# Optimization experiments

Measured on AMD Instinct MI355X. Metric: run time of the kernel, lower is better.

The kernel has to match this reference:

```python
import jax, jax.numpy as jnp
import numpy as np

B, N, C = 64, 8192, 64
C4 = C // 4
EPS_BN = 1e-5


def setup_inputs() -> dict:
    key = jax.random.key(0)
    ks = jax.random.split(key, 12)
    s = 0.05
    return {
        "x": jax.random.normal(ks[0], (B, N, 10), jnp.float32),
        "y": jax.random.normal(ks[1], (B, N, 13), jnp.float32),
        "W_l": jax.random.normal(ks[2], (10, C), jnp.float32) * s,
        "b_l": jax.random.normal(ks[3], (C,), jnp.float32) * s,
        "W_r": jax.random.normal(ks[4], (13, C), jnp.float32) * s,
        "b_r": jax.random.normal(ks[5], (C,), jnp.float32) * s,
        "W_qk": jax.random.normal(ks[6], (C4, C), jnp.float32) * s,  # shared q/k 1x1-conv weight
        "W_v": jax.random.normal(ks[7], (C, C), jnp.float32) * s,
        "b_v": jax.random.normal(ks[8], (C,), jnp.float32) * s,
        "W_t": jax.random.normal(ks[9], (C, C), jnp.float32) * s,
        "b_t": jax.random.normal(ks[10], (C,), jnp.float32) * s,
        "gamma": jnp.ones((C,), jnp.float32),
        "beta": jnp.zeros((C,), jnp.float32),
    }


def reference(x, y, W_l, b_l, W_r, b_r, W_qk, W_v, b_v, W_t, b_t, gamma, beta):
    # x: [B,N,10] -> linear_l; y: [B,N,13] -> linear_r  (torch keeps [B,C,N]; we keep [B,N,C])
    X = x @ W_l + b_l                                   # [B,N,C]
    Y = y @ W_r + b_r                                   # [B,N,C]
    # 1x1 convs == per-point matmuls; attention runs ACROSS the batch dim per point n
    xq = jnp.einsum('bnc,dc->nbd', X, W_qk)             # [N,B,C/4]
    yk = jnp.einsum('bnc,dc->nbd', Y, W_qk)             # [N,B,C/4] (shared weight)
    yv = jnp.einsum('bnc,dc->nbd', Y, W_v) + b_v        # [N,B,C]
    energy = jnp.einsum('nbd,ned->nbe', xq, yk)         # [N,B,B]
    attn = jax.nn.softmax(energy, axis=-1)
    # extra L1 renormalization over dim=1 (offset-attention style)
    attn = attn / (1e-9 + attn.sum(axis=1, keepdims=True))
    yr = jnp.einsum('nbe,nec->bnc', attn, yv)           # [B,N,C]
    # trans_conv -> BatchNorm (training-mode batch stats) -> ReLU -> residual -> max over points
    t = jnp.einsum('bnc,dc->bnd', X - yr, W_t) + b_t    # [B,N,C]
    mean = t.mean(axis=(0, 1))
    var = t.var(axis=(0, 1))                            # biased var, as BN uses
    tn = gamma * (t - mean) * jax.lax.rsqrt(var + EPS_BN) + beta
    xres = X + jax.nn.relu(tn)                          # [B,N,C]
    return jnp.max(xres, axis=1)[:, :, None]            # [B,C,1] to match torch layout
```

## Files before the change

### kernel.cpp

```cpp
#include <hip/hip_runtime.h>
#include <hip/hip_bf16.h>

#define B_ 64
#define N_ 8192
#define C_ 64

using short8 = __attribute__((ext_vector_type(8))) short;
using f32x4  = __attribute__((ext_vector_type(4))) float;

#define MFMA16(a, b, c) __builtin_amdgcn_mfma_f32_16x16x32_bf16((a), (b), (c), 0, 0, 0)

__device__ inline unsigned short f2bf(float f) {
  union { float f; unsigned int u; } v; v.f = f;
  unsigned int r = v.u + 0x7FFFu + ((v.u >> 16) & 1u);
  return (unsigned short)(r >> 16);
}


__global__ void k0_prep(const float* __restrict__ W_l, const float* __restrict__ b_l,
                        const float* __restrict__ W_r, const float* __restrict__ b_r,
                        const float* __restrict__ W_qk, const float* __restrict__ W_v,
                        const float* __restrict__ b_v, const float* __restrict__ W_t,
                        float* __restrict__ wsf) {
  const int tid = threadIdx.x;
  float* b_lq_ = wsf + 33920;
  float* b_rk_ = wsf + 33936;
  float* b_rv_ = wsf + 33952;
  unsigned short* wb = (unsigned short*)(wsf + 34016);
  unsigned short* BLQ = wb;
  unsigned short* BRK = wb + 512;
  unsigned short* BL  = wb + 1024;
  unsigned short* BRV = wb + 3072;
  unsigned short* BT  = wb + 5120;
  if (blockIdx.x == 0) {
    for (int i = tid; i < 512; i += 256) {
      int d = i >> 5, kk = i & 31;
      unsigned short o = 0;
      if (kk < 10) {
        float s = 0.f;
        for (int c = 0; c < 64; ++c) s = fmaf(W_l[kk * 64 + c], W_qk[d * 64 + c], s);
        o = f2bf(s);
      }
      BLQ[i] = o;
    }
    for (int i = tid; i < 512; i += 256) {
      int d = i >> 5, kk = i & 31, k = kk - 16;
      unsigned short o = 0;
      if (k >= 0 && k < 13) {
        float s = 0.f;
        for (int c = 0; c < 64; ++c) s = fmaf(W_r[k * 64 + c], W_qk[d * 64 + c], s);
        o = f2bf(s);
      }
      BRK[i] = o;
    }
    if (tid < 32) {
      int d = tid & 15;
      const float* bb = (tid < 16) ? b_l : b_r;
      float s = 0.f;
      for (int c = 0; c < 64; ++c) s = fmaf(bb[c], W_qk[d * 64 + c], s);
      ((tid < 16) ? b_lq_ : b_rk_)[d] = s;
    }
  } else if (blockIdx.x == 1) {
    for (int i = tid; i < 2048; i += 256) {
      int c = i >> 5, kk = i & 31, k = kk - 16;
      unsigned short o = 0;
      if (k >= 0 && k < 13) {
        float s = 0.f;
        for (int j = 0; j < 64; ++j) s = fmaf(W_r[k * 64 + j], W_v[c * 64 + j], s);
        o = f2bf(s);
      }
      BRV[i] = o;
    }
    if (tid < 64) {
      float s = b_v[tid];
      for (int j = 0; j < 64; ++j) s = fmaf(b_r[j], W_v[tid * 64 + j], s);
      b_rv_[tid] = s;
    }
  } else if (blockIdx.x == 2) {
    for (int i = tid; i < 2048; i += 256) {
      int c = i >> 5, kk = i & 31;
      BL[i] = (kk < 10) ? f2bf(W_l[kk * 64 + c]) : (unsigned short)0;
    }
    for (int i = tid; i < 1024; i += 256) wsf[i] = 0.f;
  } else {
    for (int i = tid; i < 4096; i += 256) BT[i] = f2bf(W_t[i]);
  }
}

__global__ __launch_bounds__(256, 4)
void k1_attn(const float* __restrict__ x, const float* __restrict__ y,
             const float* __restrict__ wsf,
             const float* __restrict__ b_l, const float* __restrict__ b_t,
             float* __restrict__ stats) {
  __shared__ __align__(16) short Axy[64 * 40];
  __shared__ __align__(16) short xkA[64 * 24];
  __shared__ __align__(16) short ykB[64 * 24];
  __shared__ __align__(16) short yvT[64 * 72];
  __shared__ __align__(16) short aZ[4 * 2304];
  __shared__ float scr[512];

  const float* b_lq_ = wsf + 33920;
  const float* b_rk_ = wsf + 33936;
  const float* b_rv_ = wsf + 33952;
  const unsigned short* wbase = (const unsigned short*)(wsf + 34016);
  const unsigned short* BLQ = wbase;
  const unsigned short* BRK = wbase + 512;
  const unsigned short* BL  = wbase + 1024;
  const unsigned short* BRV = wbase + 3072;
  const unsigned short* BT  = wbase + 5120;
  unsigned short* tg = (unsigned short*)(wsf + 34016) + 9216;

  const int n    = blockIdx.x;
  const int tid  = threadIdx.x;
  const int w    = tid >> 6;
  const int lane = tid & 63;
  const int l15  = lane & 15;
  const int q    = lane >> 4;
  const int r0   = w * 16;
  short* const aw = aZ + w * 2304;
  short* const Zw = aw + 1152;

  {
    const int b = tid >> 2, i = tid & 3;
    const float* xp = x + ((size_t)b * N_ + n) * 10;
    const float* yp = y + ((size_t)b * N_ + n) * 13;
    short* Ar = Axy + b * 40;
    Ar[i]      = (short)f2bf(xp[i]);
    Ar[i + 4]  = (short)f2bf(xp[i + 4]);
    Ar[i + 8]  = (i + 8 < 10) ? (short)f2bf(xp[i + 8]) : (short)0;
    Ar[12 + i] = 0;
    Ar[16 + i]      = (short)f2bf(yp[i]);
    Ar[20 + i]      = (short)f2bf(yp[i + 4]);
    Ar[24 + i]      = (short)f2bf(yp[i + 8]);
    Ar[28 + i]      = (i + 12 < 13) ? (short)f2bf(yp[i + 12]) : (short)0;
  }
  __syncthreads();

  const short8 aA = *(const short8*)&Axy[(r0 + l15) * 40 + q * 8];

  f32x4 xq, yk, X[4], yv[4];
  {
    const short8 bq = *(const short8*)&BLQ[l15 * 32 + q * 8];
    const float bl1 = b_lq_[l15];
    xq = MFMA16(aA, bq, ((f32x4){bl1, bl1, bl1, bl1}));
    const short8 bk = *(const short8*)&BRK[l15 * 32 + q * 8];
    const float bk1 = b_rk_[l15];
    yk = MFMA16(aA, bk, ((f32x4){bk1, bk1, bk1, bk1}));
  }
#pragma unroll
  for (int f = 0; f < 4; ++f) {
    const int c = f * 16 + l15;
    const short8 bl = *(const short8*)&BL[c * 32 + q * 8];
    const float bX = b_l[c];
    X[f] = MFMA16(aA, bl, ((f32x4){bX, bX, bX, bX}));
    const short8 bv = *(const short8*)&BRV[c * 32 + q * 8];
    const float bV = b_rv_[c];
    yv[f] = MFMA16(aA, bv, ((f32x4){bV, bV, bV, bV}));
  }
#pragma unroll
  for (int j = 0; j < 4; ++j) {
    xkA[(r0 + q * 4 + j) * 24 + l15] = (short)f2bf(xq[j]);
    ykB[(r0 + q * 4 + j) * 24 + l15] = (short)f2bf(yk[j]);
  }
#pragma unroll
  for (int f = 0; f < 4; ++f)
#pragma unroll
    for (int j = 0; j < 4; ++j)
      yvT[(f * 16 + l15) * 72 + (r0 + q * 4 + j)] = (short)f2bf(yv[f][j]);
  __syncthreads();

  const short8 z8 = (short8)(short)0;
  const short8 aq = (q < 2) ? *(const short8*)&xkA[(r0 + l15) * 24 + q * 8] : z8;
  f32x4 E[4];
#pragma unroll
  for (int f = 0; f < 4; ++f) {
    const short8 bk = (q < 2) ? *(const short8*)&ykB[(f * 16 + l15) * 24 + q * 8] : z8;
    E[f] = MFMA16(aq, bk, ((f32x4){0.f, 0.f, 0.f, 0.f}));
  }

  float inv_r[4];
#pragma unroll
  for (int j = 0; j < 4; ++j) {
    float s = 0.f;
#pragma unroll
    for (int f = 0; f < 4; ++f) { E[f][j] = __expf(E[f][j]); s += E[f][j]; }
    s += __shfl_xor(s, 1);
    s += __shfl_xor(s, 2);
    s += __shfl_xor(s, 4);
    s += __shfl_xor(s, 8);
    inv_r[j] = 1.0f / s;
  }
#pragma unroll
  for (int f = 0; f < 4; ++f) {
    float cs = E[f][0] * inv_r[0] + E[f][1] * inv_r[1] + E[f][2] * inv_r[2] + E[f][3] * inv_r[3];
    cs += __shfl_xor(cs, 16);
    cs += __shfl_xor(cs, 32);
    if (lane < 16) scr[w * 64 + f * 16 + l15] = cs;
  }
  __syncthreads();
  float csvv[4];
#pragma unroll
  for (int f = 0; f < 4; ++f) {
    const int col = f * 16 + l15;
    csvv[f] = 1.0f / (1e-9f + scr[col] + scr[64 + col] + scr[128 + col] + scr[192 + col]);
  }
#pragma unroll
  for (int f = 0; f < 4; ++f)
#pragma unroll
    for (int j = 0; j < 4; ++j)
      aw[(q * 4 + j) * 72 + f * 16 + l15] = (short)f2bf(E[f][j] * inv_r[j] * csvv[f]);

  const short8 aA0 = *(const short8*)&aw[l15 * 72 + q * 8];
  const short8 aA1 = *(const short8*)&aw[l15 * 72 + 32 + q * 8];
#pragma unroll
  for (int f = 0; f < 4; ++f) {
    const short8 b0 = *(const short8*)&yvT[(f * 16 + l15) * 72 + q * 8];
    const short8 b1 = *(const short8*)&yvT[(f * 16 + l15) * 72 + 32 + q * 8];
    f32x4 yr = MFMA16(aA0, b0, ((f32x4){0.f, 0.f, 0.f, 0.f}));
    yr = MFMA16(aA1, b1, yr);
#pragma unroll
    for (int j = 0; j < 4; ++j)
      Zw[(q * 4 + j) * 72 + f * 16 + l15] = (short)f2bf(X[f][j] - yr[j]);
  }

  const short8 aZ0 = *(const short8*)&Zw[l15 * 72 + q * 8];
  const short8 aZ1 = *(const short8*)&Zw[l15 * 72 + 32 + q * 8];
  unsigned short* tp = tg + (size_t)n * 4096;
  f32x4 t[4];
#pragma unroll
  for (int f = 0; f < 4; ++f) {
    const int c = f * 16 + l15;
    const short8 bt0 = *(const short8*)&BT[c * 64 + q * 8];
    const short8 bt1 = *(const short8*)&BT[c * 64 + 32 + q * 8];
    const float bT = b_t[c];
    t[f] = MFMA16(aZ0, bt0, ((f32x4){bT, bT, bT, bT}));
    t[f] = MFMA16(aZ1, bt1, t[f]);
#pragma unroll
    for (int j = 0; j < 4; ++j)
      tp[(r0 + q * 4 + j) * 64 + c] = f2bf(t[f][j]);
  }
  __syncthreads();
#pragma unroll
  for (int f = 0; f < 4; ++f) {
    float s = 0.f, ss = 0.f;
#pragma unroll
    for (int j = 0; j < 4; ++j) { s += t[f][j]; ss = fmaf(t[f][j], t[f][j], ss); }
    s  += __shfl_xor(s, 16);  s  += __shfl_xor(s, 32);
    ss += __shfl_xor(ss, 16); ss += __shfl_xor(ss, 32);
    if (lane < 16) {
      scr[w * 64 + f * 16 + l15]       = s;
      scr[256 + w * 64 + f * 16 + l15] = ss;
    }
  }
  __syncthreads();
  if (tid < 64) {
    const float s  = scr[tid] + scr[64 + tid] + scr[128 + tid] + scr[192 + tid];
    const float ss = scr[256 + tid] + scr[320 + tid] + scr[384 + tid] + scr[448 + tid];
    float* st = stats + (n & 7) * 128;
    atomicAdd(&st[tid], s);
    atomicAdd(&st[64 + tid], ss);
  }
}

__global__ void k2_stats(const float* __restrict__ stats, float* __restrict__ meanr) {
  const int c = threadIdx.x;
  if (c < 64) {
    float s = 0.f, ss = 0.f;
    for (int r = 0; r < 8; ++r) { s += stats[r * 128 + c]; ss += stats[r * 128 + 64 + c]; }
    const float inv = 1.0f / (float)(B_ * N_);
    const float mu = s * inv;
    const float var = fmaf(ss, inv, -mu * mu);
    meanr[c] = mu;
    meanr[64 + c] = rsqrtf(var + 1e-5f);
  }
}

__global__ __launch_bounds__(256)
void k3_max(const float* __restrict__ x, const float* __restrict__ W_l,
            const float* __restrict__ b_l, const float* __restrict__ gamma,
            const float* __restrict__ beta, const unsigned short* __restrict__ tg,
            const float* __restrict__ meanr, float* __restrict__ pmax)
{
  const int b = blockIdx.x >> 3;
  const int chunk = blockIdx.x & 7;
  const int c = threadIdx.x & 63;
  const int sub = threadIdx.x >> 6;
  float wl[10];
#pragma unroll
  for (int k = 0; k < 10; ++k) wl[k] = W_l[k * 64 + c];
  const float bl = b_l[c];
  const float g = gamma[c], be = beta[c];
  const float mu = meanr[c], rs = meanr[64 + c];
  float m = -1e30f;
  const int nbase = chunk * 1024 + sub;
  for (int j = 0; j < 256; ++j) {
    const int n = nbase + j * 4;
    const float* xp = x + ((size_t)b * N_ + n) * 10;
    float X = bl;
#pragma unroll
    for (int k = 0; k < 10; ++k) X = fmaf(xp[k], wl[k], X);
    union { unsigned int u; float f; } tv;
    tv.u = ((unsigned int)tg[(size_t)n * 4096 + b * 64 + c]) << 16;
    const float tn = fmaf(g * (tv.f - mu), rs, be);
    m = fmaxf(m, X + fmaxf(tn, 0.f));
  }
  __shared__ float sm[4][64];
  sm[sub][c] = m;
  __syncthreads();
  if (threadIdx.x < 64) {
    const float r = fmaxf(fmaxf(sm[0][c], sm[1][c]), fmaxf(sm[2][c], sm[3][c]));
    pmax[(size_t)blockIdx.x * 64 + c] = r;
  }
}

__global__ void k4_final(const float* __restrict__ pmax, float* __restrict__ out) {
  const int b = blockIdx.x, c = threadIdx.x;
  float m = -1e30f;
  for (int ch = 0; ch < 8; ++ch) m = fmaxf(m, pmax[((size_t)b * 8 + ch) * 64 + c]);
  out[b * 64 + c] = m;
}

extern "C" void kernel_launch(void* const* d_in, const int* in_sizes, int n_in,
                              void* d_out, int out_size, void* d_ws, size_t ws_size,
                              hipStream_t stream) {
  const float* x     = (const float*)d_in[0];
  const float* y     = (const float*)d_in[1];
  const float* W_l   = (const float*)d_in[2];
  const float* b_l   = (const float*)d_in[3];
  const float* W_r   = (const float*)d_in[4];
  const float* b_r   = (const float*)d_in[5];
  const float* W_qk  = (const float*)d_in[6];
  const float* W_v   = (const float*)d_in[7];
  const float* b_v   = (const float*)d_in[8];
  const float* W_t   = (const float*)d_in[9];
  const float* b_t   = (const float*)d_in[10];
  const float* gamma = (const float*)d_in[11];
  const float* beta  = (const float*)d_in[12];
  float* out = (float*)d_out;

  float* wsf = (float*)d_ws;
  float* stats = wsf;
  float* meanr = wsf + 1024;
  float* pmax  = wsf + 1152;
  unsigned short* tg = (unsigned short*)(wsf + 34016) + 9216;

  hipLaunchKernelGGL(k0_prep, dim3(4), dim3(256), 0, stream,
                     W_l, b_l, W_r, b_r, W_qk, W_v, b_v, W_t, wsf);
  hipLaunchKernelGGL(k1_attn, dim3(N_), dim3(256), 0, stream,
                     x, y, wsf, b_l, b_t, stats);
  hipLaunchKernelGGL(k2_stats, dim3(1), dim3(64), 0, stream, stats, meanr);
  hipLaunchKernelGGL(k3_max, dim3(512), dim3(256), 0, stream,
                     x, W_l, b_l, gamma, beta, tg, meanr, pmax);
  hipLaunchKernelGGL(k4_final, dim3(64), dim3(64), 0, stream, pmax, out);
}
```

Measured before the change: 248.9 us.

## Fold q/k weights into bilinear matrix, reassociate value path, transpose t layout

The attention kernel now computes the energy through a precomputed bilinear matrix (W_l·W_qk)(W_r·W_qk)^T with biases folded in as a ones column. The value path is reassociated as (attn·Y)·(W_r W_v) instead of materialising yv, which removes several MFMAs and LDS transposes. The t buffer is stored batch-major so the max kernel can read contiguous vectorized bf16 runs, and that kernel processes four channels per lane with folded BN constants over twice as many blocks. It also switches to cheaper round-half-up bf16 conversion and raises the occupancy hint, at the cost of slightly different rounding and extra bf16 quantisation of intermediate products.

```diff
diff --git a/kernel.cpp b/kernel.cpp
--- a/kernel.cpp
+++ b/kernel.cpp
@@ -1,9 +1,7 @@
 #include <hip/hip_runtime.h>
-#include <hip/hip_bf16.h>
 
 #define B_ 64
 #define N_ 8192
-#define C_ 64
 
 using short8 = __attribute__((ext_vector_type(8))) short;
 using f32x4  = __attribute__((ext_vector_type(4))) float;
@@ -12,8 +10,11 @@
 
 __device__ inline unsigned short f2bf(float f) {
   union { float f; unsigned int u; } v; v.f = f;
-  unsigned int r = v.u + 0x7FFFu + ((v.u >> 16) & 1u);
-  return (unsigned short)(r >> 16);
+  return (unsigned short)((v.u + 0x8000u) >> 16);
+}
+__device__ inline float bf2f(unsigned int hi16_in_low) {
+  union { unsigned int u; float f; } v; v.u = hi16_in_low << 16;
+  return v.f;
 }
 
 
@@ -23,63 +24,60 @@
                         const float* __restrict__ b_v, const float* __restrict__ W_t,
                         float* __restrict__ wsf) {
   const int tid = threadIdx.x;
-  float* b_lq_ = wsf + 33920;
-  float* b_rk_ = wsf + 33936;
-  float* b_rv_ = wsf + 33952;
-  unsigned short* wb = (unsigned short*)(wsf + 34016);
-  unsigned short* BLQ = wb;
-  unsigned short* BRK = wb + 512;
-  unsigned short* BL  = wb + 1024;
-  unsigned short* BRV = wb + 3072;
-  unsigned short* BT  = wb + 5120;
+  unsigned short* wb   = (unsigned short*)(wsf + 66688);
+  unsigned short* BM   = wb;
+  unsigned short* BL   = wb + 512;
+  unsigned short* BRV2 = wb + 2560;
+  unsigned short* BT   = wb + 4608;
   if (blockIdx.x == 0) {
-    for (int i = tid; i < 512; i += 256) {
-      int d = i >> 5, kk = i & 31;
+    __shared__ float Wlq[11 * 16], Wrk[14 * 16];
+    for (int idx = tid; idx < 11 * 16; idx += 256) {
+      int i = idx >> 4, d = idx & 15;
+      const float* a = (i < 10) ? (W_l + i * 64) : b_l;
+      float s = 0.f;
+      for (int c = 0; c < 64; ++c) s = fmaf(a[c], W_qk[d * 64 + c], s);
+      Wlq[idx] = s;
+    }
+    for (int idx = tid; idx < 14 * 16; idx += 256) {
+      int j = idx >> 4, d = idx & 15;
+      const float* a = (j < 13) ? (W_r + j * 64) : b_r;
+      float s = 0.f;
+      for (int c = 0; c < 64; ++c) s = fmaf(a[c], W_qk[d * 64 + c], s);
+      Wrk[idx] = s;
+    }
+    __syncthreads();
+    for (int idx = tid; idx < 512; idx += 256) {
+      int j = idx >> 5, kk = idx & 31;
       unsigned short o = 0;
-      if (kk < 10) {
+      if (j < 14 && kk < 11) {
         float s = 0.f;
-        for (int c = 0; c < 64; ++c) s = fmaf(W_l[kk * 64 + c], W_qk[d * 64 + c], s);
+        for (int d = 0; d < 16; ++d) s = fmaf(Wlq[kk * 16 + d], Wrk[j * 16 + d], s);
         o = f2bf(s);
       }
-      BLQ[i] = o;
-    }
-    for (int i = tid; i < 512; i += 256) {
-      int d = i >> 5, kk = i & 31, k = kk - 16;
+      BM[idx] = o;
+    }
+  } else if (blockIdx.x == 1) {
+    for (int idx = tid; idx < 2048; idx += 256) {
+      int c = idx >> 5, kk = idx & 31;
       unsigned short o = 0;
-      if (k >= 0 && k < 13) {
+      if (kk < 13) {
         float s = 0.f;
-        for (int c = 0; c < 64; ++c) s = fmaf(W_r[k * 64 + c], W_qk[d * 64 + c], s);
+        for (int j = 0; j < 64; ++j) s = fmaf(W_r[kk * 64 + j], W_v[c * 64 + j], s);
+        o = f2bf(s);
+      } else if (kk == 13) {
+        float s = b_v[c];
+        for (int j = 0; j < 64; ++j) s = fmaf(b_r[j], W_v[c * 64 + j], s);
         o = f2bf(s);
       }
-      BRK[i] = o;
-    }
-    if (tid < 32) {
-      int d = tid & 15;
-      const float* bb = (tid < 16) ? b_l : b_r;
-      float s = 0.f;
-      for (int c = 0; c < 64; ++c) s = fmaf(bb[c], W_qk[d * 64 + c], s);
-      ((tid < 16) ? b_lq_ : b_rk_)[d] = s;
-    }
-  } else if (blockIdx.x == 1) {
-    for (int i = tid; i < 2048; i += 256) {
-      int c = i >> 5, kk = i & 31, k = kk - 16;
+      BRV2[idx] = o;
+    }
+  } else if (blockIdx.x == 2) {
+    for (int idx = tid; idx < 2048; idx += 256) {
+      int c = idx >> 5, kk = idx & 31;
       unsigned short o = 0;
-      if (k >= 0 && k < 13) {
-        float s = 0.f;
-        for (int j = 0; j < 64; ++j) s = fmaf(W_r[k * 64 + j], W_v[c * 64 + j], s);
-        o = f2bf(s);
-      }
-      BRV[i] = o;
-    }
-    if (tid < 64) {
-      float s = b_v[tid];
-      for (int j = 0; j < 64; ++j) s = fmaf(b_r[j], W_v[tid * 64 + j], s);
-      b_rv_[tid] = s;
-    }
-  } else if (blockIdx.x == 2) {
-    for (int i = tid; i < 2048; i += 256) {
-      int c = i >> 5, kk = i & 31;
-      BL[i] = (kk < 10) ? f2bf(W_l[kk * 64 + c]) : (unsigned short)0;
+      if (kk < 10) o = f2bf(W_l[kk * 64 + c]);
+      else if (kk == 10) o = f2bf(b_l[c]);
+      BL[idx] = o;
     }
     for (int i = tid; i < 1024; i += 256) wsf[i] = 0.f;
   } else {
@@ -87,28 +85,22 @@
   }
 }
 
-__global__ __launch_bounds__(256, 4)
+__global__ __launch_bounds__(256, 6)
 void k1_attn(const float* __restrict__ x, const float* __restrict__ y,
-             const float* __restrict__ wsf,
-             const float* __restrict__ b_l, const float* __restrict__ b_t,
+             const float* __restrict__ wsf, const float* __restrict__ b_t,
              float* __restrict__ stats) {
   __shared__ __align__(16) short Axy[64 * 40];
-  __shared__ __align__(16) short xkA[64 * 24];
-  __shared__ __align__(16) short ykB[64 * 24];
-  __shared__ __align__(16) short yvT[64 * 72];
-  __shared__ __align__(16) short aZ[4 * 2304];
+  __shared__ __align__(16) short YT[16 * 72];
+  __shared__ __align__(16) short awZ[4 * 1152];
+  __shared__ __align__(16) short GU[4 * 256];
   __shared__ float scr[512];
 
-  const float* b_lq_ = wsf + 33920;
-  const float* b_rk_ = wsf + 33936;
-  const float* b_rv_ = wsf + 33952;
-  const unsigned short* wbase = (const unsigned short*)(wsf + 34016);
-  const unsigned short* BLQ = wbase;
-  const unsigned short* BRK = wbase + 512;
-  const unsigned short* BL  = wbase + 1024;
-  const unsigned short* BRV = wbase + 3072;
-  const unsigned short* BT  = wbase + 5120;
-  unsigned short* tg = (unsigned short*)(wsf + 34016) + 9216;
+  const unsigned short* wb   = (const unsigned short*)(wsf + 66688);
+  const unsigned short* BM   = wb;
+  const unsigned short* BL   = wb + 512;
+  const unsigned short* BRV2 = wb + 2560;
+  const unsigned short* BT   = wb + 4608;
+  unsigned short* tg = (unsigned short*)(wsf + 66688) + 8704;
 
   const int n    = blockIdx.x;
   const int tid  = threadIdx.x;
@@ -117,65 +109,53 @@
   const int l15  = lane & 15;
   const int q    = lane >> 4;
   const int r0   = w * 16;
-  short* const aw = aZ + w * 2304;
-  short* const Zw = aw + 1152;
+  short* const aw = awZ + w * 1152;
+  short* const gu = GU + w * 256;
 
   {
     const int b = tid >> 2, i = tid & 3;
     const float* xp = x + ((size_t)b * N_ + n) * 10;
     const float* yp = y + ((size_t)b * N_ + n) * 13;
     short* Ar = Axy + b * 40;
-    Ar[i]      = (short)f2bf(xp[i]);
-    Ar[i + 4]  = (short)f2bf(xp[i + 4]);
-    Ar[i + 8]  = (i + 8 < 10) ? (short)f2bf(xp[i + 8]) : (short)0;
-    Ar[12 + i] = 0;
-    Ar[16 + i]      = (short)f2bf(yp[i]);
-    Ar[20 + i]      = (short)f2bf(yp[i + 4]);
-    Ar[24 + i]      = (short)f2bf(yp[i + 8]);
-    Ar[28 + i]      = (i + 12 < 13) ? (short)f2bf(yp[i + 12]) : (short)0;
-  }
-  __syncthreads();
-
+    Ar[i]     = (short)f2bf(xp[i]);
+    Ar[i + 4] = (short)f2bf(xp[i + 4]);
+    short v8 = 0;
+    if (i < 2) v8 = (short)f2bf(xp[i + 8]);
+    else if (i == 2) v8 = (short)0x3F80;
+    Ar[i + 8]  = v8;
+    Ar[i + 12] = 0;
+    const short y0 = (short)f2bf(yp[i]);
+    const short y1 = (short)f2bf(yp[i + 4]);
+    const short y2 = (short)f2bf(yp[i + 8]);
+    short y3 = 0;
+    if (i == 0) y3 = (short)f2bf(yp[12]);
+    else if (i == 1) y3 = (short)0x3F80;
+    Ar[16 + i] = y0;  Ar[20 + i] = y1;  Ar[24 + i] = y2;  Ar[28 + i] = y3;
+    YT[i * 72 + b] = y0;  YT[(i + 4) * 72 + b] = y1;
+    YT[(i + 8) * 72 + b] = y2;  YT[(i + 12) * 72 + b] = y3;
+  }
+  __syncthreads();
+
+  const short8 z8 = {0, 0, 0, 0, 0, 0, 0, 0};
+  const f32x4 zero4 = {0.f, 0.f, 0.f, 0.f};
   const short8 aA = *(const short8*)&Axy[(r0 + l15) * 40 + q * 8];
 
-  f32x4 xq, yk, X[4], yv[4];
-  {
-    const short8 bq = *(const short8*)&BLQ[l15 * 32 + q * 8];
-    const float bl1 = b_lq_[l15];
-    xq = MFMA16(aA, bq, ((f32x4){bl1, bl1, bl1, bl1}));
-    const short8 bk = *(const short8*)&BRK[l15 * 32 + q * 8];
-    const float bk1 = b_rk_[l15];
-    yk = MFMA16(aA, bk, ((f32x4){bk1, bk1, bk1, bk1}));
-  }
-#pragma unroll
-  for (int f = 0; f < 4; ++f) {
-    const int c = f * 16 + l15;
-    const short8 bl = *(const short8*)&BL[c * 32 + q * 8];
-    const float bX = b_l[c];
-    X[f] = MFMA16(aA, bl, ((f32x4){bX, bX, bX, bX}));
-    const short8 bv = *(const short8*)&BRV[c * 32 + q * 8];
-    const float bV = b_rv_[c];
-    yv[f] = MFMA16(aA, bv, ((f32x4){bV, bV, bV, bV}));
-  }
-#pragma unroll
-  for (int j = 0; j < 4; ++j) {
-    xkA[(r0 + q * 4 + j) * 24 + l15] = (short)f2bf(xq[j]);
-    ykB[(r0 + q * 4 + j) * 24 + l15] = (short)f2bf(yk[j]);
-  }
+  f32x4 G = MFMA16(aA, *(const short8*)&BM[l15 * 32 + q * 8], zero4);
+  f32x4 X[4];
 #pragma unroll
   for (int f = 0; f < 4; ++f)
-#pragma unroll
-    for (int j = 0; j < 4; ++j)
-      yvT[(f * 16 + l15) * 72 + (r0 + q * 4 + j)] = (short)f2bf(yv[f][j]);
-  __syncthreads();
-
-  const short8 z8 = (short8)(short)0;
-  const short8 aq = (q < 2) ? *(const short8*)&xkA[(r0 + l15) * 24 + q * 8] : z8;
+    X[f] = MFMA16(aA, *(const short8*)&BL[(f * 16 + l15) * 32 + q * 8], zero4);
+#pragma unroll
+  for (int j = 0; j < 4; ++j) gu[(q * 4 + j) * 16 + l15] = (short)f2bf(G[j]);
+
+  short8 aG = z8;
+  if (q < 2) aG = *(const short8*)&gu[l15 * 16 + q * 8];
   f32x4 E[4];
 #pragma unroll
   for (int f = 0; f < 4; ++f) {
-    const short8 bk = (q < 2) ? *(const short8*)&ykB[(f * 16 + l15) * 24 + q * 8] : z8;
-    E[f] = MFMA16(aq, bk, ((f32x4){0.f, 0.f, 0.f, 0.f}));
+    short8 bk = z8;
+    if (q < 2) bk = *(const short8*)&Axy[(f * 16 + l15) * 40 + 16 + q * 8];
+    E[f] = MFMA16(aG, bk, zero4);
   }
 
   float inv_r[4];
@@ -212,32 +192,34 @@
 
   const short8 aA0 = *(const short8*)&aw[l15 * 72 + q * 8];
   const short8 aA1 = *(const short8*)&aw[l15 * 72 + 32 + q * 8];
-#pragma unroll
-  for (int f = 0; f < 4; ++f) {
-    const short8 b0 = *(const short8*)&yvT[(f * 16 + l15) * 72 + q * 8];
-    const short8 b1 = *(const short8*)&yvT[(f * 16 + l15) * 72 + 32 + q * 8];
-    f32x4 yr = MFMA16(aA0, b0, ((f32x4){0.f, 0.f, 0.f, 0.f}));
-    yr = MFMA16(aA1, b1, yr);
+
+  f32x4 U = MFMA16(aA0, *(const short8*)&YT[l15 * 72 + q * 8], zero4);
+  U = MFMA16(aA1, *(const short8*)&YT[l15 * 72 + 32 + q * 8], U);
+#pragma unroll
+  for (int j = 0; j < 4; ++j) gu[(q * 4 + j) * 16 + l15] = (short)f2bf(U[j]);
+  short8 aU = z8;
+  if (q < 2) aU = *(const short8*)&gu[l15 * 16 + q * 8];
+
+#pragma unroll
+  for (int f = 0; f < 4; ++f) {
+    f32x4 yr = MFMA16(aU, *(const short8*)&BRV2[(f * 16 + l15) * 32 + q * 8], zero4);
 #pragma unroll
     for (int j = 0; j < 4; ++j)
-      Zw[(q * 4 + j) * 72 + f * 16 + l15] = (short)f2bf(X[f][j] - yr[j]);
-  }
-
-  const short8 aZ0 = *(const short8*)&Zw[l15 * 72 + q * 8];
-  const short8 aZ1 = *(const short8*)&Zw[l15 * 72 + 32 + q * 8];
-  unsigned short* tp = tg + (size_t)n * 4096;
+      aw[(q * 4 + j) * 72 + f * 16 + l15] = (short)f2bf(X[f][j] - yr[j]);
+  }
+
+  const short8 aZ0 = *(const short8*)&aw[l15 * 72 + q * 8];
+  const short8 aZ1 = *(const short8*)&aw[l15 * 72 + 32 + q * 8];
   f32x4 t[4];
 #pragma unroll
   for (int f = 0; f < 4; ++f) {
     const int c = f * 16 + l15;
-    const short8 bt0 = *(const short8*)&BT[c * 64 + q * 8];
-    const short8 bt1 = *(const short8*)&BT[c * 64 + 32 + q * 8];
     const float bT = b_t[c];
-    t[f] = MFMA16(aZ0, bt0, ((f32x4){bT, bT, bT, bT}));
-    t[f] = MFMA16(aZ1, bt1, t[f]);
+    t[f] = MFMA16(aZ0, *(const short8*)&BT[c * 64 + q * 8], ((f32x4){bT, bT, bT, bT}));
+    t[f] = MFMA16(aZ1, *(const short8*)&BT[c * 64 + 32 + q * 8], t[f]);
 #pragma unroll
     for (int j = 0; j < 4; ++j)
-      tp[(r0 + q * 4 + j) * 64 + c] = f2bf(t[f][j]);
+      tg[(size_t)(r0 + q * 4 + j) * (N_ * 64) + (size_t)n * 64 + c] = f2bf(t[f][j]);
   }
   __syncthreads();
 #pragma unroll
@@ -281,42 +263,63 @@
             const float* __restrict__ beta, const unsigned short* __restrict__ tg,
             const float* __restrict__ meanr, float* __restrict__ pmax)
 {
-  const int b = blockIdx.x >> 3;
-  const int chunk = blockIdx.x & 7;
-  const int c = threadIdx.x & 63;
-  const int sub = threadIdx.x >> 6;
-  float wl[10];
-#pragma unroll
-  for (int k = 0; k < 10; ++k) wl[k] = W_l[k * 64 + c];
-  const float bl = b_l[c];
-  const float g = gamma[c], be = beta[c];
-  const float mu = meanr[c], rs = meanr[64 + c];
-  float m = -1e30f;
-  const int nbase = chunk * 1024 + sub;
-  for (int j = 0; j < 256; ++j) {
-    const int n = nbase + j * 4;
+  const int b = blockIdx.x >> 4;
+  const int chunk = blockIdx.x & 15;
+  const int wv = threadIdx.x >> 6;
+  const int lane = threadIdx.x & 63;
+  const int c0 = (lane & 15) * 4;
+  const int nsub = lane >> 4;
+  float4 wl4[10];
+#pragma unroll
+  for (int k = 0; k < 10; ++k) wl4[k] = *(const float4*)&W_l[k * 64 + c0];
+  const float4 bl  = *(const float4*)&b_l[c0];
+  const float4 g   = *(const float4*)&gamma[c0];
+  const float4 be  = *(const float4*)&beta[c0];
+  const float4 mu  = *(const float4*)&meanr[c0];
+  const float4 rs  = *(const float4*)&meanr[64 + c0];
+  float4 grs, bmb;
+  grs.x = g.x * rs.x; grs.y = g.y * rs.y; grs.z = g.z * rs.z; grs.w = g.w * rs.w;
+  bmb.x = be.x - mu.x * grs.x; bmb.y = be.y - mu.y * grs.y;
+  bmb.z = be.z - mu.z * grs.z; bmb.w = be.w - mu.w * grs.w;
+  float4 m = {-1e30f, -1e30f, -1e30f, -1e30f};
+  const size_t tgb = (size_t)b << 19;
+  const int n0 = chunk * 512 + wv * 128 + nsub;
+  for (int jj = 0; jj < 32; ++jj) {
+    const int n = n0 + jj * 4;
+    const uint2 tv = *(const uint2*)&tg[tgb + (size_t)n * 64 + c0];
     const float* xp = x + ((size_t)b * N_ + n) * 10;
-    float X = bl;
-#pragma unroll
-    for (int k = 0; k < 10; ++k) X = fmaf(xp[k], wl[k], X);
-    union { unsigned int u; float f; } tv;
-    tv.u = ((unsigned int)tg[(size_t)n * 4096 + b * 64 + c]) << 16;
-    const float tn = fmaf(g * (tv.f - mu), rs, be);
-    m = fmaxf(m, X + fmaxf(tn, 0.f));
-  }
+    float4 X = bl;
+#pragma unroll
+    for (int k = 0; k < 10; ++k) {
+      const float xk = xp[k];
+      X.x = fmaf(xk, wl4[k].x, X.x); X.y = fmaf(xk, wl4[k].y, X.y);
+      X.z = fmaf(xk, wl4[k].z, X.z); X.w = fmaf(xk, wl4[k].w, X.w);
+    }
+    const float t0 = bf2f(tv.x & 0xFFFFu), t1 = bf2f(tv.x >> 16);
+    const float t2 = bf2f(tv.y & 0xFFFFu), t3 = bf2f(tv.y >> 16);
+    m.x = fmaxf(m.x, X.x + fmaxf(fmaf(t0, grs.x, bmb.x), 0.f));
+    m.y = fmaxf(m.y, X.y + fmaxf(fmaf(t1, grs.y, bmb.y), 0.f));
+    m.z = fmaxf(m.z, X.z + fmaxf(fmaf(t2, grs.z, bmb.z), 0.f));
+    m.w = fmaxf(m.w, X.w + fmaxf(fmaf(t3, grs.w, bmb.w), 0.f));
+  }
+  m.x = fmaxf(m.x, __shfl_xor(m.x, 16)); m.y = fmaxf(m.y, __shfl_xor(m.y, 16));
+  m.z = fmaxf(m.z, __shfl_xor(m.z, 16)); m.w = fmaxf(m.w, __shfl_xor(m.w, 16));
+  m.x = fmaxf(m.x, __shfl_xor(m.x, 32)); m.y = fmaxf(m.y, __shfl_xor(m.y, 32));
+  m.z = fmaxf(m.z, __shfl_xor(m.z, 32)); m.w = fmaxf(m.w, __shfl_xor(m.w, 32));
   __shared__ float sm[4][64];
-  sm[sub][c] = m;
+  if (lane < 16) *(float4*)&sm[wv][c0] = m;
   __syncthreads();
   if (threadIdx.x < 64) {
-    const float r = fmaxf(fmaxf(sm[0][c], sm[1][c]), fmaxf(sm[2][c], sm[3][c]));
-    pmax[(size_t)blockIdx.x * 64 + c] = r;
+    const float r = fmaxf(fmaxf(sm[0][threadIdx.x], sm[1][threadIdx.x]),
+                          fmaxf(sm[2][threadIdx.x], sm[3][threadIdx.x]));
+    pmax[(size_t)blockIdx.x * 64 + threadIdx.x] = r;
   }
 }
 
 __global__ void k4_final(const float* __restrict__ pmax, float* __restrict__ out) {
   const int b = blockIdx.x, c = threadIdx.x;
   float m = -1e30f;
-  for (int ch = 0; ch < 8; ++ch) m = fmaxf(m, pmax[((size_t)b * 8 + ch) * 64 + c]);
+  for (int ch = 0; ch < 16; ++ch) m = fmaxf(m, pmax[((size_t)b * 16 + ch) * 64 + c]);
   out[b * 64 + c] = m;
 }
 
@@ -342,14 +345,14 @@
   float* stats = wsf;
   float* meanr = wsf + 1024;
   float* pmax  = wsf + 1152;
-  unsigned short* tg = (unsigned short*)(wsf + 34016) + 9216;
+  const unsigned short* tg = (const unsigned short*)(wsf + 66688) + 8704;
 
   hipLaunchKernelGGL(k0_prep, dim3(4), dim3(256), 0, stream,
                      W_l, b_l, W_r, b_r, W_qk, W_v, b_v, W_t, wsf);
   hipLaunchKernelGGL(k1_attn, dim3(N_), dim3(256), 0, stream,
-                     x, y, wsf, b_l, b_t, stats);
+                     x, y, wsf, b_t, stats);
   hipLaunchKernelGGL(k2_stats, dim3(1), dim3(64), 0, stream, stats, meanr);
-  hipLaunchKernelGGL(k3_max, dim3(512), dim3(256), 0, stream,
+  hipLaunchKernelGGL(k3_max, dim3(1024), dim3(256), 0, stream,
                      x, W_l, b_l, gamma, beta, tg, meanr, pmax);
   hipLaunchKernelGGL(k4_final, dim3(64), dim3(64), 0, stream, pmax, out);
 }
```

Result: faster. 208.6 us (-16.2%).
